# Kernel optimization log

Hardware: AMD Instinct MI355X
Metric: run time of the kernel (lower is better)

## Reference

```python
import jax, jax.numpy as jnp
import numpy as np
from jax import lax

LEAK = 0.01   # nn.LeakyReLU default negative slope
EPS = 1e-5    # BatchNorm2d eps


def _conv(x, w, b, stride, pad):
    # torch Conv2d, NCHW / OIHW
    y = lax.conv_general_dilated(x, w, (stride, stride), [(pad, pad), (pad, pad)],
                                 dimension_numbers=('NCHW', 'OIHW', 'NCHW'))
    return y + b[None, :, None, None]


def _bn_lrelu(x, g, b):
    # BatchNorm2d in training mode (torch default): batch statistics over (N,H,W)
    m = jnp.mean(x, axis=(0, 2, 3), keepdims=True)
    v = jnp.var(x, axis=(0, 2, 3), keepdims=True)
    xn = (x - m) * lax.rsqrt(v + EPS) * g[None, :, None, None] + b[None, :, None, None]
    return jnp.where(xn >= 0, xn, LEAK * xn)


def _convt(x, w, b):
    # ConvTranspose2d with stride == kernel_size, padding=0: non-overlapping
    # k x k expansion of every pixel -> expressible as one einsum + reshape.
    # w: (Cin, Cout, k, k) (torch ConvTranspose2d layout)
    B, C, H, W = x.shape
    _, Co, k, _ = w.shape
    y = jnp.einsum('bchw,coij->bohiwj', x, w).reshape(B, Co, H * k, W * k)
    return y + b[None, :, None, None]


def setup_inputs() -> dict:
    key = jax.random.key(0)
    ks = iter(jax.random.split(key, 64))
    def rn(shape, s=0.05):
        return jax.random.normal(next(ks), shape, dtype=jnp.float32) * s
    d = {}
    d['x'] = jax.random.normal(next(ks), (16, 3, 128, 128), dtype=jnp.float32)
    enc_shapes = [(64, 3, 4, 4), (128, 64, 4, 4), (256, 128, 4, 4), (256, 256, 4, 4)]
    for i, s in enumerate(enc_shapes):
        d[f'enc_w{i}'] = rn(s)
        d[f'enc_b{i}'] = jnp.zeros((s[0],), jnp.float32)
    for i, c in enumerate([64, 128, 256]):
        d[f'ebn_g{i}'] = jnp.ones((c,), jnp.float32)
        d[f'ebn_b{i}'] = jnp.zeros((c,), jnp.float32)
    d['codebook'] = rn((512, 256), 1.0)  # (codebook_size, latent_dim)
    dec_shapes = [(256, 128, 4, 4), (128, 64, 2, 2), (64, 32, 2, 2)]
    for i, s in enumerate(dec_shapes):
        d[f'dec_w{i}'] = rn(s)
        d[f'dec_b{i}'] = jnp.zeros((s[1],), jnp.float32)
        d[f'dbn_g{i}'] = jnp.ones((s[1],), jnp.float32)
        d[f'dbn_b{i}'] = jnp.zeros((s[1],), jnp.float32)
    d['dec_w3'] = rn((3, 32, 1, 1))
    d['dec_b3'] = jnp.zeros((3,), jnp.float32)
    return d


def reference(x,
              enc_w0, enc_b0, ebn_g0, ebn_b0,
              enc_w1, enc_b1, ebn_g1, ebn_b1,
              enc_w2, enc_b2, ebn_g2, ebn_b2,
              enc_w3, enc_b3,
              codebook,
              dec_w0, dec_b0, dbn_g0, dbn_b0,
              dec_w1, dec_b1, dbn_g1, dbn_b1,
              dec_w2, dec_b2, dbn_g2, dbn_b2,
              dec_w3, dec_b3):
    # ---- encoder ----
    h = _bn_lrelu(_conv(x, enc_w0, enc_b0, 2, 1), ebn_g0, ebn_b0)   # (B,64,64,64)
    h = _bn_lrelu(_conv(h, enc_w1, enc_b1, 2, 1), ebn_g1, ebn_b1)   # (B,128,32,32)
    h = _bn_lrelu(_conv(h, enc_w2, enc_b2, 2, 1), ebn_g2, ebn_b2)   # (B,256,16,16)
    z = _conv(h, enc_w3, enc_b3, 2, 1)                               # (B,256,8,8)

    # ---- vector quantizer ----
    B, C, H, W = z.shape
    zf = z.transpose(0, 2, 3, 1).reshape(-1, C)                      # (BHW, C)
    # squared L2 distances to every codebook entry
    d2 = (jnp.sum(zf * zf, axis=-1, keepdims=True)
          - 2.0 * zf @ codebook.T
          + jnp.sum(codebook * codebook, axis=-1)[None, :])          # (BHW, K)
    idx = jnp.argmin(d2, axis=-1)                                    # (BHW,)
    min_d = jnp.min(d2, axis=-1)
    q = codebook[idx]                                                # (BHW, C)
    commitment_loss = jnp.mean((lax.stop_gradient(q) - zf) ** 2)
    codebook_loss = jnp.mean((q - lax.stop_gradient(zf)) ** 2)
    q_st = zf + lax.stop_gradient(q - zf)                            # straight-through
    qz = q_st.reshape(B, H, W, C).transpose(0, 3, 1, 2)              # (B,256,8,8)

    # ---- decoder ----
    h = _bn_lrelu(_convt(qz, dec_w0, dec_b0), dbn_g0, dbn_b0)        # (B,128,32,32)
    h = _bn_lrelu(_convt(h, dec_w1, dec_b1), dbn_g1, dbn_b1)         # (B,64,64,64)
    h = _bn_lrelu(_convt(h, dec_w2, dec_b2), dbn_g2, dbn_b2)         # (B,32,128,128)
    out = jnp.tanh(jnp.einsum('bchw,oc->bohw', h, dec_w3[:, :, 0, 0])
                   + dec_b3[None, :, None, None])                    # (B,3,128,128)

    return (out, commitment_loss, codebook_loss,
            idx.reshape(B, H, W), min_d.reshape(B, H, W))
```

## Files before the change

### kernel.cpp

```cpp
#include <hip/hip_runtime.h>
#include <math.h>

#define LEAK 0.01f

typedef __bf16 bf16x8 __attribute__((ext_vector_type(8)));
typedef float f32x4 __attribute__((ext_vector_type(4)));
typedef unsigned short ushort;
typedef unsigned int uint32;

struct HL { ushort h, l; };

__device__ inline HL split_bf16(float x) {
    unsigned u = __float_as_uint(x);
    unsigned hr = (u + 0x7FFFu + ((u >> 16) & 1u)) >> 16;
    float fh = __uint_as_float(hr << 16);
    float r = x - fh;
    unsigned v = __float_as_uint(r);
    unsigned lr = (v + 0x7FFFu + ((v >> 16) & 1u)) >> 16;
    HL out; out.h = (ushort)hr; out.l = (ushort)lr;
    return out;
}

template<int MODE>
__device__ inline void stage_load(float (&pv)[2][4], const float* __restrict__ Bf,
                                  int kbase, int n0, int tid,
                                  int Ci, int Hin, int Ho, int lgHo, int lgHW) {
#pragma unroll
    for (int r = 0; r < 2; ++r) {
        int g = r * 256 + tid;
        int nl = g >> 3, kg = g & 7;
        int n = n0 + nl;
        if (MODE == 0) {
            int k4 = kbase + (kg << 2);
            int ic = k4 >> 4, kh = (k4 >> 2) & 3;
            int ow = n & (Ho - 1), oh = (n >> lgHo) & (Ho - 1), b = n >> (lgHo + lgHo);
            int ih = oh * 2 - 1 + kh;
            int ihc = ih < 0 ? 0 : (ih >= Hin ? Hin - 1 : ih);
            int iwb = ow * 2 - 1;
            size_t base = ((size_t)(b * Ci + ic) * Hin + ihc) * Hin;
#pragma unroll
            for (int e = 0; e < 4; ++e) {
                int iw = iwb + e;
                int iwc = iw < 0 ? 0 : (iw >= Hin ? Hin - 1 : iw);
                pv[r][e] = Bf[base + iwc];
            }
        } else {
            int c = kbase + (kg << 2);
            int b = n >> lgHW, hw = n & ((1 << lgHW) - 1);
            size_t base = (((size_t)(b * Ci + c)) << lgHW) + hw;
            size_t str = (size_t)1 << lgHW;
#pragma unroll
            for (int e = 0; e < 4; ++e) pv[r][e] = Bf[base + e * str];
        }
    }
}

template<int MODE>
__global__ __launch_bounds__(256, 3) void gemm_mfma(
    const ushort* __restrict__ Ah, const ushort* __restrict__ Al,
    const float* __restrict__ Bf,
    const float* __restrict__ bnt, const float* __restrict__ gamma,
    const float* __restrict__ beta, float invN, int chanShift,
    const float* __restrict__ bias, float* __restrict__ P,
    int Mtiles, int Ntiles, int K, int Kslice, int KS, int outSize,
    int Ci, int Hin, int Co, int Ho, int lgHo,
    int lgHW, int lgHin, int lgCo, int lgk,
    float* __restrict__ statsBnt)
{
    __shared__ __align__(16) uint32 Bsp[64 * 36];
    __shared__ float scs[256], shs[256];

    int bid = blockIdx.x;
    int ntile = bid % Ntiles; bid /= Ntiles;
    int mtile = bid % Mtiles;
    int ks = bid / Mtiles;
    int tid = threadIdx.x;
    int lane = tid & 63, w = tid >> 6;
    int quad = lane >> 4, tl = lane & 15;
    int n0 = ntile << 6, m0 = mtile << 7, k0 = ks * Kslice;
    int Kt = K >> 5;

    bool useBN = (bnt != nullptr);
    int c0 = k0 >> chanShift;
    if (useBN) {
        int nch = Kslice >> chanShift;
        for (int c = tid; c < nch; c += 256) {
            float m = bnt[(c0 + c) * 2] * invN;
            float var = bnt[(c0 + c) * 2 + 1] * invN - m * m;
            float scale = gamma[c0 + c] * rsqrtf(var + 1e-5f);
            scs[c] = scale;
            shs[c] = beta[c0 + c] - m * scale;
        }
    }
    __syncthreads();

    f32x4 zero4 = {0.f, 0.f, 0.f, 0.f};
    f32x4 acc[2][4];
#pragma unroll
    for (int mt = 0; mt < 2; ++mt)
#pragma unroll
        for (int nt = 0; nt < 4; ++nt) acc[mt][nt] = zero4;

    float pv[2][4];
    stage_load<MODE>(pv, Bf, k0, n0, tid, Ci, Hin, Ho, lgHo, lgHW);

    for (int kc = 0; kc < Kslice; kc += 32) {
        int kbase = k0 + kc;
        int kt = kbase >> 5;
#pragma unroll
        for (int r = 0; r < 2; ++r) {
            int g = r * 256 + tid;
            int nl = g >> 3, kg = g & 7;
            int k4 = kbase + (kg << 2);
            uint32 pk[4];
            if (MODE == 0) {
                int ic = k4 >> 4, kh = (k4 >> 2) & 3;
                int n = n0 + nl;
                int ow = n & (Ho - 1), oh = (n >> lgHo) & (Ho - 1);
                int ih = oh * 2 - 1 + kh;
                bool rowok = (unsigned)ih < (unsigned)Hin;
                int iwb = ow * 2 - 1;
                float sc_ = useBN ? scs[ic - c0] : 0.f;
                float sh_ = useBN ? shs[ic - c0] : 0.f;
#pragma unroll
                for (int e = 0; e < 4; ++e) {
                    int iw = iwb + e;
                    bool ok = rowok && ((unsigned)iw < (unsigned)Hin);
                    float f = pv[r][e];
                    if (useBN) { f = f * sc_ + sh_; f = f >= 0.f ? f : LEAK * f; }
                    if (!ok) f = 0.f;
                    HL s = split_bf16(f);
                    pk[e] = ((uint32)s.h << 16) | s.l;
                }
            } else {
#pragma unroll
                for (int e = 0; e < 4; ++e) {
                    float f = pv[r][e];
                    if (useBN) {
                        int lc = k4 + e - k0;
                        f = f * scs[lc] + shs[lc];
                        f = f >= 0.f ? f : LEAK * f;
                    }
                    HL s = split_bf16(f);
                    pk[e] = ((uint32)s.h << 16) | s.l;
                }
            }
            *(uint4*)&Bsp[nl * 36 + (kg << 2)] = make_uint4(pk[0], pk[1], pk[2], pk[3]);
        }
        __syncthreads();

        bool more = (kc + 32) < Kslice;
        float pvn[2][4];
        if (more) stage_load<MODE>(pvn, Bf, kbase + 32, n0, tid, Ci, Hin, Ho, lgHo, lgHW);

        bf16x8 afh[2], afl[2];
#pragma unroll
        for (int mt = 0; mt < 2; ++mt) {
            int mtAbs = (m0 >> 4) + (w << 1) + mt;
            size_t abase = (((size_t)mtAbs * Kt + kt) << 6) + lane;
            afh[mt] = *(const bf16x8*)(Ah + abase * 8);
            afl[mt] = *(const bf16x8*)(Al + abase * 8);
        }
        bf16x8 bfh[4], bfl[4];
#pragma unroll
        for (int nt = 0; nt < 4; ++nt) {
            int base = ((nt << 4) + tl) * 36 + (quad << 3);
            uint4 ua = *(const uint4*)&Bsp[base];
            uint4 ub = *(const uint4*)&Bsp[base + 4];
            union { uint32 u[4]; bf16x8 v; } H, L;
            H.u[0] = __builtin_amdgcn_perm(ua.y, ua.x, 0x07060302u);
            H.u[1] = __builtin_amdgcn_perm(ua.w, ua.z, 0x07060302u);
            H.u[2] = __builtin_amdgcn_perm(ub.y, ub.x, 0x07060302u);
            H.u[3] = __builtin_amdgcn_perm(ub.w, ub.z, 0x07060302u);
            L.u[0] = __builtin_amdgcn_perm(ua.y, ua.x, 0x05040100u);
            L.u[1] = __builtin_amdgcn_perm(ua.w, ua.z, 0x05040100u);
            L.u[2] = __builtin_amdgcn_perm(ub.y, ub.x, 0x05040100u);
            L.u[3] = __builtin_amdgcn_perm(ub.w, ub.z, 0x05040100u);
            bfh[nt] = H.v; bfl[nt] = L.v;
        }
#pragma unroll
        for (int mt = 0; mt < 2; ++mt)
#pragma unroll
            for (int nt = 0; nt < 4; ++nt) {
                acc[mt][nt] = __builtin_amdgcn_mfma_f32_16x16x32_bf16(afh[mt], bfh[nt], acc[mt][nt], 0, 0, 0);
                acc[mt][nt] = __builtin_amdgcn_mfma_f32_16x16x32_bf16(afh[mt], bfl[nt], acc[mt][nt], 0, 0, 0);
                acc[mt][nt] = __builtin_amdgcn_mfma_f32_16x16x32_bf16(afl[mt], bfh[nt], acc[mt][nt], 0, 0, 0);
            }
        __syncthreads();
        if (more) {
#pragma unroll
            for (int r = 0; r < 2; ++r)
#pragma unroll
                for (int e = 0; e < 4; ++e) pv[r][e] = pvn[r][e];
        }
    }

    float* dst = P + (size_t)ks * outSize;
    if (MODE == 0) {
#pragma unroll
        for (int nt = 0; nt < 4; ++nt) {
            int n = n0 + (nt << 4) + tl;
            int ow = n & (Ho - 1), oh = (n >> lgHo) & (Ho - 1), b = n >> (lgHo + lgHo);
#pragma unroll
            for (int mt = 0; mt < 2; ++mt) {
                int mb = m0 + (w << 5) + (mt << 4) + (quad << 2);
#pragma unroll
                for (int r = 0; r < 4; ++r) {
                    int oc = mb + r;
                    float v = acc[mt][nt][r];
                    if (KS == 1) v += bias[oc];
                    dst[((size_t)(b * Co + oc) * Ho + oh) * Ho + ow] = v;
                }
            }
        }
    } else {
        bool doStats = (statsBnt != nullptr);
        if (doStats) {
            if (tid < 2 * Co) scs[tid] = 0.f;
            __syncthreads();
        }
        int kf = 1 << lgk;
        int Ho2 = Hin << lgk;
        float ssum[2][4] = {{0.f,0.f,0.f,0.f},{0.f,0.f,0.f,0.f}};
        float ssq [2][4] = {{0.f,0.f,0.f,0.f},{0.f,0.f,0.f,0.f}};
#pragma unroll
        for (int nt = 0; nt < 4; ++nt) {
            int n = n0 + (nt << 4) + tl;
            int b = n >> lgHW, hw = n & ((1 << lgHW) - 1);
            int h = hw >> lgHin, wp = hw & (Hin - 1);
#pragma unroll
            for (int mt = 0; mt < 2; ++mt) {
                int mb = m0 + (w << 5) + (mt << 4) + (quad << 2);
#pragma unroll
                for (int r = 0; r < 4; ++r) {
                    int m = mb + r;
                    int o = m & (Co - 1), ij = m >> lgCo;
                    int ii = ij >> lgk, jj = ij & (kf - 1);
                    float v = acc[mt][nt][r];
                    if (KS == 1) v += bias[o];
                    if (doStats) { ssum[mt][r] += v; ssq[mt][r] += v * v; }
                    dst[((size_t)(b * Co + o) * Ho2 + (h << lgk) + ii) * Ho2 + (wp << lgk) + jj] = v;
                }
            }
        }
        if (doStats) {
#pragma unroll
            for (int mt = 0; mt < 2; ++mt)
#pragma unroll
                for (int r = 0; r < 4; ++r) {
                    float s = ssum[mt][r], q2 = ssq[mt][r];
#pragma unroll
                    for (int m2 = 1; m2 < 16; m2 <<= 1) {
                        s  += __shfl_xor(s,  m2);
                        q2 += __shfl_xor(q2, m2);
                    }
                    if (tl == 0) {
                        int m = m0 + (w << 5) + (mt << 4) + (quad << 2) + r;
                        int o = m & (Co - 1);
                        atomicAdd(&scs[o * 2],     s);
                        atomicAdd(&scs[o * 2 + 1], q2);
                    }
                }
            __syncthreads();
            if (tid < 2 * Co) atomicAdd(&statsBnt[tid], scs[tid]);
        }
    }
}

__device__ inline int fragaddr(int m, int k, int K) {
    return ((((m >> 4) * (K >> 5) + (k >> 5)) << 9) | (((k >> 3) & 3) << 7) | ((m & 15) << 3) | (k & 7));
}

#define OUT_CL   786432
#define OUT_CB   786433
#define OUT_IDX  786434
#define OUT_MIND 787458

__global__ void prologue(const float* __restrict__ w1, const float* __restrict__ w2,
                         const float* __restrict__ w3, const float* __restrict__ d0,
                         const float* __restrict__ d1, const float* __restrict__ d2,
                         ushort* __restrict__ WH, ushort* __restrict__ WL,
                         const float* __restrict__ cb, float* __restrict__ cbT,
                         float* __restrict__ bnt, float* __restrict__ dout) {
    int blk = blockIdx.x;
    int tid = threadIdx.x;
    if (blk < 24) {
        bnt[blk * 256 + tid] = 0.f;
        if (blk == 0 && tid < 2) dout[OUT_CL + tid] = 0.f;
        return;
    }
    if (blk < 536) {
        int idx = (blk - 24) * 256 + tid;
        int k = idx & 511, c = idx >> 9;
        cbT[idx] = cb[k * 256 + c];
        return;
    }
    int idx = (blk - 536) * 256 + tid;
    if (idx >= 2269184) return;
    float v; int dst;
    if (idx < 131072) {
        int m = idx >> 10, k = idx & 1023;
        v = w1[idx];
        dst = fragaddr(m, k, 1024);
    } else if (idx < 655360) {
        int i = idx - 131072;
        int m = i >> 11, k = i & 2047;
        v = w2[i];
        dst = 131072 + fragaddr(m, k, 2048);
    } else if (idx < 1703936) {
        int i = idx - 655360;
        int m = i >> 12, k = i & 4095;
        v = w3[i];
        dst = 655360 + fragaddr(m, k, 4096);
    } else if (idx < 2228224) {
        int i = idx - 1703936;
        int m = i >> 8, c = i & 255;
        int o = m & 127, ij = m >> 7;
        v = d0[((size_t)c * 128 + o) * 16 + ij];
        dst = 1703936 + fragaddr(m, c, 256);
    } else if (idx < 2260992) {
        int i = idx - 2228224;
        int m = i >> 7, c = i & 127;
        int o = m & 63, ij = m >> 6;
        v = d1[((size_t)c * 64 + o) * 4 + ij];
        dst = 2228224 + fragaddr(m, c, 128);
    } else {
        int i = idx - 2260992;
        int m = i >> 6, c = i & 63;
        int o = m & 31, ij = m >> 5;
        v = d2[((size_t)c * 32 + o) * 4 + ij];
        dst = 2260992 + fragaddr(m, c, 64);
    }
    HL s = split_bf16(v);
    WH[dst] = s.h; WL[dst] = s.l;
}

template<int OCT>
__global__ __launch_bounds__(256) void conv4x4(
    const float* __restrict__ x, const float* __restrict__ w,
    const float* __restrict__ bias, float* __restrict__ P,
    float* __restrict__ bnt,
    int B, int Ci, int Hin, int Co, int Ho)
{
    __shared__ float cst[4][2 * OCT];
    int ogn = Co / OCT;
    int ntile = (B * Ho * Ho) >> 8;
    int bid = blockIdx.x;
    int tile = bid % ntile; bid /= ntile;
    int og = bid % ogn;
    int oc0 = og * OCT;

    int px = (tile << 8) + threadIdx.x;
    int ow = px % Ho; int t = px / Ho;
    int oh = t % Ho;  int b = t / Ho;

    int off[16]; float fm[16];
    int ih0 = oh * 2 - 1, iw0 = ow * 2 - 1;
#pragma unroll
    for (int kh = 0; kh < 4; ++kh)
#pragma unroll
        for (int kw = 0; kw < 4; ++kw) {
            int ih = ih0 + kh, iw = iw0 + kw;
            bool ok = (ih >= 0) && (ih < Hin) && (iw >= 0) && (iw < Hin);
            int ihc = ih < 0 ? 0 : (ih >= Hin ? Hin - 1 : ih);
            int iwc = iw < 0 ? 0 : (iw >= Hin ? Hin - 1 : iw);
            off[kh * 4 + kw] = ihc * Hin + iwc;
            fm[kh * 4 + kw] = ok ? 1.f : 0.f;
        }

    float acc[OCT];
#pragma unroll
    for (int u = 0; u < OCT; ++u) acc[u] = bias[oc0 + u];

    const float* xc = x + (size_t)b * Ci * Hin * Hin;
    const float* wi = w + (size_t)oc0 * Ci * 16;
    int HinHin = Hin * Hin;
    for (int ic = 0; ic < Ci; ++ic) {
        float xv[16];
#pragma unroll
        for (int q = 0; q < 16; ++q) xv[q] = xc[off[q]] * fm[q];
#pragma unroll
        for (int u = 0; u < OCT; ++u) {
            const float* wo = wi + (size_t)u * Ci * 16;
            float a = acc[u];
#pragma unroll
            for (int q = 0; q < 16; ++q) a += xv[q] * wo[q];
            acc[u] = a;
        }
        xc += HinHin;
        wi += 16;
    }
    size_t obase = (((size_t)b * Co + oc0) * Ho + oh) * Ho + ow;
    size_t opl = (size_t)Ho * Ho;
#pragma unroll
    for (int u = 0; u < OCT; ++u) P[obase + u * opl] = acc[u];

    float sv[OCT], qv[OCT];
#pragma unroll
    for (int u = 0; u < OCT; ++u) { sv[u] = acc[u]; qv[u] = acc[u] * acc[u]; }
#pragma unroll
    for (int m2 = 1; m2 < 64; m2 <<= 1)
#pragma unroll
        for (int u = 0; u < OCT; ++u) {
            sv[u] += __shfl_xor(sv[u], m2);
            qv[u] += __shfl_xor(qv[u], m2);
        }
    int lane = threadIdx.x & 63, wv = threadIdx.x >> 6;
    if (lane == 0) {
#pragma unroll
        for (int u = 0; u < OCT; ++u) { cst[wv][u * 2] = sv[u]; cst[wv][u * 2 + 1] = qv[u]; }
    }
    __syncthreads();
    if (threadIdx.x < 2 * OCT) {
        float v = cst[0][threadIdx.x] + cst[1][threadIdx.x] + cst[2][threadIdx.x] + cst[3][threadIdx.x];
        atomicAdd(&bnt[(oc0 + (threadIdx.x >> 1)) * 2 + (threadIdx.x & 1)], v);
    }
}

__global__ void reduce_bias4(const float4* __restrict__ P, const float* __restrict__ bias,
                             float4* __restrict__ y, int outSize4, int KS, int Co, int HW4) {
    int i = blockIdx.x * 256 + threadIdx.x;
    if (i >= outSize4) return;
    float bv = bias[(i / HW4) % Co];
    float4 s = make_float4(bv, bv, bv, bv);
    for (int ks = 0; ks < KS; ++ks) {
        float4 p = P[(size_t)ks * outSize4 + i];
        s.x += p.x; s.y += p.y; s.z += p.z; s.w += p.w;
    }
    y[i] = s;
}

__global__ void reduce_bias_stats4(const float4* __restrict__ P, const float* __restrict__ bias,
                                   float4* __restrict__ y, float* __restrict__ bnt,
                                   int outSize4, int KS, int Co, int HW4, int nch) {
    int tid = threadIdx.x;
    int i = blockIdx.x * 256 + tid;
    int c = (i / HW4) % Co;
    float bv = bias[c];
    float4 s = make_float4(bv, bv, bv, bv);
    for (int ks = 0; ks < KS; ++ks) {
        float4 p = P[(size_t)ks * outSize4 + i];
        s.x += p.x; s.y += p.y; s.z += p.z; s.w += p.w;
    }
    y[i] = s;
    float ls  = s.x + s.y + s.z + s.w;
    float ls2 = s.x * s.x + s.y * s.y + s.z * s.z + s.w * s.w;
    __shared__ float as[16], aq[16];
    if (tid < 16) { as[tid] = 0.f; aq[tid] = 0.f; }
    __syncthreads();
    int c0 = ((blockIdx.x * 256) / HW4) % Co;
    atomicAdd(&as[c - c0], ls);
    atomicAdd(&aq[c - c0], ls2);
    __syncthreads();
    if (tid < nch) {
        atomicAdd(&bnt[(c0 + tid) * 2],     as[tid]);
        atomicAdd(&bnt[(c0 + tid) * 2 + 1], aq[tid]);
    }
}

__global__ void vq_main(const float* __restrict__ z, const float* __restrict__ cbT,
                        const float* __restrict__ cb,
                        float* __restrict__ q, float* __restrict__ dout) {
    int r0 = blockIdx.x * 4;
    int tid = threadIdx.x;
    int lane = tid & 63, w = tid >> 6;

    __shared__ __align__(16) float zT[256][4];
    __shared__ float wred[4][4];
    __shared__ float zn2s[4];
    __shared__ float wbd[4][4];
    __shared__ int   wbi[4][4];
    __shared__ int   bestsh[4];
    __shared__ float bestd[4];

    int b = r0 >> 6, s0 = r0 & 63;
    float4 zv = *(const float4*)&z[((size_t)(b * 256 + tid)) * 64 + s0];
    *(float4*)&zT[tid][0] = zv;

    float p0 = zv.x * zv.x, p1 = zv.y * zv.y, p2 = zv.z * zv.z, p3 = zv.w * zv.w;
#pragma unroll
    for (int m2 = 1; m2 < 64; m2 <<= 1) {
        p0 += __shfl_xor(p0, m2); p1 += __shfl_xor(p1, m2);
        p2 += __shfl_xor(p2, m2); p3 += __shfl_xor(p3, m2);
    }
    if (lane == 0) { wred[w][0] = p0; wred[w][1] = p1; wred[w][2] = p2; wred[w][3] = p3; }
    __syncthreads();
    if (tid < 4) zn2s[tid] = wred[0][tid] + wred[1][tid] + wred[2][tid] + wred[3][tid];
    __syncthreads();

    float d0[4], d1[4];
#pragma unroll
    for (int rr = 0; rr < 4; ++rr) { d0[rr] = 0.f; d1[rr] = 0.f; }
    float cn0 = 0.f, cn1 = 0.f;
#pragma unroll 4
    for (int c = 0; c < 256; ++c) {
        float cv0 = cbT[c * 512 + tid];
        float cv1 = cbT[c * 512 + 256 + tid];
        cn0 += cv0 * cv0;
        cn1 += cv1 * cv1;
        float4 za = *(const float4*)&zT[c][0];
        d0[0] += za.x * cv0; d1[0] += za.x * cv1;
        d0[1] += za.y * cv0; d1[1] += za.y * cv1;
        d0[2] += za.z * cv0; d1[2] += za.z * cv1;
        d0[3] += za.w * cv0; d1[3] += za.w * cv1;
    }

#pragma unroll
    for (int rr = 0; rr < 4; ++rr) {
        float dist0 = zn2s[rr] - 2.f * d0[rr] + cn0;
        float dist1 = zn2s[rr] - 2.f * d1[rr] + cn1;
        float bd = dist0; int bi = tid;
        if (dist1 < bd) { bd = dist1; bi = tid + 256; }
#pragma unroll
        for (int m2 = 1; m2 < 64; m2 <<= 1) {
            float od = __shfl_xor(bd, m2); int oi = __shfl_xor(bi, m2);
            if (od < bd || (od == bd && oi < bi)) { bd = od; bi = oi; }
        }
        if (lane == 0) { wbd[w][rr] = bd; wbi[w][rr] = bi; }
    }
    __syncthreads();
    if (tid < 4) {
        float bd = wbd[0][tid]; int bi = wbi[0][tid];
#pragma unroll
        for (int ww = 1; ww < 4; ++ww) {
            float od = wbd[ww][tid]; int oi = wbi[ww][tid];
            if (od < bd || (od == bd && oi < bi)) { bd = od; bi = oi; }
        }
        bestsh[tid] = bi; bestd[tid] = bd;
        dout[OUT_IDX + r0 + tid]  = (float)bi;
        dout[OUT_MIND + r0 + tid] = bd;
    }
    __syncthreads();

    float4 qv;
    qv.x = cb[(size_t)bestsh[0] * 256 + tid];
    qv.y = cb[(size_t)bestsh[1] * 256 + tid];
    qv.z = cb[(size_t)bestsh[2] * 256 + tid];
    qv.w = cb[(size_t)bestsh[3] * 256 + tid];
    *(float4*)&q[((size_t)(b * 256 + tid)) * 64 + s0] = qv;
    if (tid == 0) {
        float ls = (bestd[0] + bestd[1] + bestd[2] + bestd[3]) * (1.f / 262144.f);
        atomicAdd(&dout[OUT_CL], ls);
        atomicAdd(&dout[OUT_CB], ls);
    }
}

__global__ void final_conv_tanh(const float* __restrict__ hbuf, const float* __restrict__ bnt,
                                const float* __restrict__ g, const float* __restrict__ bt,
                                const float* __restrict__ w3, const float* __restrict__ b3,
                                float* __restrict__ out) {
    __shared__ float sc[32], sh[32], sw[96];
    int tid = threadIdx.x;
    if (tid < 32) {
        float m = bnt[tid * 2] * (1.f / 262144.f);
        float var = bnt[tid * 2 + 1] * (1.f / 262144.f) - m * m;
        float scale = g[tid] * rsqrtf(var + 1e-5f);
        sc[tid] = scale;
        sh[tid] = bt[tid] - m * scale;
    }
    if (tid < 96) sw[tid] = w3[tid];
    __syncthreads();
    int idx = blockIdx.x * 256 + tid;
    int hw4 = idx & 4095;
    int b   = idx >> 12;
    const float4* hp = (const float4*)hbuf + ((size_t)b * 32) * 4096 + hw4;
    float b0 = b3[0], b1 = b3[1], b2 = b3[2];
    float4 a0 = make_float4(b0, b0, b0, b0);
    float4 a1 = make_float4(b1, b1, b1, b1);
    float4 a2 = make_float4(b2, b2, b2, b2);
#pragma unroll 8
    for (int c = 0; c < 32; ++c) {
        float4 v = hp[(size_t)c * 4096];
        float scv = sc[c], shv = sh[c];
        float vx = v.x * scv + shv; vx = vx >= 0.f ? vx : LEAK * vx;
        float vy = v.y * scv + shv; vy = vy >= 0.f ? vy : LEAK * vy;
        float vz = v.z * scv + shv; vz = vz >= 0.f ? vz : LEAK * vz;
        float vw = v.w * scv + shv; vw = vw >= 0.f ? vw : LEAK * vw;
        float w0 = sw[c], w1 = sw[32 + c], w2 = sw[64 + c];
        a0.x += vx * w0; a0.y += vy * w0; a0.z += vz * w0; a0.w += vw * w0;
        a1.x += vx * w1; a1.y += vy * w1; a1.z += vz * w1; a1.w += vw * w1;
        a2.x += vx * w2; a2.y += vy * w2; a2.z += vz * w2; a2.w += vw * w2;
    }
    float4* op = (float4*)out;
    size_t ob = ((size_t)b * 3) * 4096 + hw4;
    op[ob]            = make_float4(tanhf(a0.x), tanhf(a0.y), tanhf(a0.z), tanhf(a0.w));
    op[ob + 4096]     = make_float4(tanhf(a1.x), tanhf(a1.y), tanhf(a1.z), tanhf(a1.w));
    op[ob + 2 * 4096] = make_float4(tanhf(a2.x), tanhf(a2.y), tanhf(a2.z), tanhf(a2.w));
}

extern "C" void kernel_launch(void* const* d_in, const int* in_sizes, int n_in,
                              void* d_out, int out_size, void* d_ws, size_t ws_size,
                              hipStream_t stream) {
    const float* x      = (const float*)d_in[0];
    const float* enc_w0 = (const float*)d_in[1];
    const float* enc_b0 = (const float*)d_in[2];
    const float* enc_w1 = (const float*)d_in[3];
    const float* enc_b1 = (const float*)d_in[4];
    const float* enc_w2 = (const float*)d_in[5];
    const float* enc_b2 = (const float*)d_in[6];
    const float* enc_w3 = (const float*)d_in[7];
    const float* enc_b3 = (const float*)d_in[8];
    const float* ebn_g0 = (const float*)d_in[9];
    const float* ebn_b0 = (const float*)d_in[10];
    const float* ebn_g1 = (const float*)d_in[11];
    const float* ebn_b1 = (const float*)d_in[12];
    const float* ebn_g2 = (const float*)d_in[13];
    const float* ebn_b2 = (const float*)d_in[14];
    const float* cb     = (const float*)d_in[15];
    const float* dec_w0 = (const float*)d_in[16];
    const float* dec_b0 = (const float*)d_in[17];
    const float* dbn_g0 = (const float*)d_in[18];
    const float* dbn_b0 = (const float*)d_in[19];
    const float* dec_w1 = (const float*)d_in[20];
    const float* dec_b1 = (const float*)d_in[21];
    const float* dbn_g1 = (const float*)d_in[22];
    const float* dbn_b1 = (const float*)d_in[23];
    const float* dec_w2 = (const float*)d_in[24];
    const float* dec_b2 = (const float*)d_in[25];
    const float* dbn_g2 = (const float*)d_in[26];
    const float* dbn_b2 = (const float*)d_in[27];
    const float* dec_w3 = (const float*)d_in[28];
    const float* dec_b3 = (const float*)d_in[29];

    float* out = (float*)d_out;
    float* ws  = (float*)d_ws;

    float*  Y0   = ws;
    float*  Y1   = ws + 4194304;
    float*  Y2   = ws + 6291456;
    float*  Z    = ws + 7340032;
    float*  Q    = ws + 7602176;
    ushort* WH   = (ushort*)(ws + 7864320);
    ushort* WL   = (ushort*)(ws + 8998912);
    float*  CBT  = ws + 10133504;
    float*  BNT  = ws + 10264576;
    float*  PART = ws + 10270720;
    float*  D0   = ws + 18659328;
    float*  D1   = ws + 20756480;
    float*  D2   = ws + 24950784;

    dim3 blk(256);

    prologue<<<9400, blk, 0, stream>>>(enc_w1, enc_w2, enc_w3, dec_w0, dec_w1, dec_w2,
                                       WH, WL, cb, CBT, BNT, out);

    conv4x4<8><<<2048, blk, 0, stream>>>(x, enc_w0, enc_b0, Y0, BNT, 16, 3, 128, 64, 64);

    gemm_mfma<0><<<512, blk, 0, stream>>>(WH, WL, Y0,
        BNT, ebn_g0, ebn_b0, 1.f / 65536.f, 4, enc_b1, PART,
        1, 256, 1024, 512, 2, 2097152, 64, 64, 128, 32, 5, 0, 0, 0, 0, nullptr);
    reduce_bias_stats4<<<2048, blk, 0, stream>>>((const float4*)PART, enc_b1, (float4*)Y1,
                                                 BNT + 1024, 524288, 2, 128, 256, 1);

    gemm_mfma<0><<<512, blk, 0, stream>>>(WH + 131072, WL + 131072, Y1,
        BNT + 1024, ebn_g1, ebn_b1, 1.f / 16384.f, 4, enc_b2, PART,
        2, 64, 2048, 512, 4, 1048576, 128, 32, 256, 16, 4, 0, 0, 0, 0, nullptr);
    reduce_bias_stats4<<<1024, blk, 0, stream>>>((const float4*)PART, enc_b2, (float4*)Y2,
                                                 BNT + 2048, 262144, 4, 256, 64, 4);

    gemm_mfma<0><<<512, blk, 0, stream>>>(WH + 655360, WL + 655360, Y2,
        BNT + 2048, ebn_g2, ebn_b2, 1.f / 4096.f, 4, enc_b3, PART,
        2, 16, 4096, 256, 16, 262144, 256, 16, 256, 8, 3, 0, 0, 0, 0, nullptr);
    reduce_bias4<<<256, blk, 0, stream>>>((const float4*)PART, enc_b3, (float4*)Z, 65536, 16, 256, 16);

    vq_main<<<256, blk, 0, stream>>>(Z, CBT, cb, Q, out);

    gemm_mfma<1><<<512, blk, 0, stream>>>(WH + 1703936, WL + 1703936, Q,
        nullptr, nullptr, nullptr, 0.f, 0, dec_b0, PART,
        16, 16, 256, 128, 2, 2097152, 256, 8, 128, 0, 0, 6, 3, 7, 2, nullptr);
    reduce_bias_stats4<<<2048, blk, 0, stream>>>((const float4*)PART, dec_b0, (float4*)D0,
                                                 BNT + 3072, 524288, 2, 128, 256, 1);

    gemm_mfma<1><<<512, blk, 0, stream>>>(WH + 2228224, WL + 2228224, D0,
        BNT + 3072, dbn_g0, dbn_b0, 1.f / 16384.f, 0, dec_b1, D1,
        2, 256, 128, 128, 1, 0, 128, 32, 64, 0, 0, 10, 5, 6, 1, BNT + 4096);

    gemm_mfma<1><<<1024, blk, 0, stream>>>(WH + 2260992, WL + 2260992, D1,
        BNT + 4096, dbn_g1, dbn_b1, 1.f / 65536.f, 0, dec_b2, D2,
        1, 1024, 64, 64, 1, 0, 64, 64, 32, 0, 0, 12, 6, 5, 1, BNT + 5120);

    final_conv_tanh<<<256, blk, 0, stream>>>(D2, BNT + 5120, dbn_g2, dbn_b2, dec_w3, dec_b3, out);
}
```

Before: 413.1 us.

## Fuse first conv into prologue and drop split-K reduce kernels

Merges the first encoder conv into the prologue launch and has it write per-tile BN partial sums instead of doing global atomics. The next GEMM reduces those partials itself. Adds an MT template so some GEMMs use 64-row M tiles without split-K and compute BN stats in their epilogue, removing two reduce_bias_stats passes. The final encoder split-K sum is folded into vq_main, which removes another reduce kernel and cuts launches and intermediate traffic. The trade-off is smaller tiles and less K-parallelism in the affected GEMMs, plus partial-sum reduction overhead in every block.

```diff
diff --git a/kernel.cpp b/kernel.cpp
--- a/kernel.cpp
+++ b/kernel.cpp
@@ -55,7 +55,7 @@
     }
 }
 
-template<int MODE>
+template<int MODE, int MT>
 __global__ __launch_bounds__(256, 3) void gemm_mfma(
     const ushort* __restrict__ Ah, const ushort* __restrict__ Al,
     const float* __restrict__ Bf,
@@ -65,7 +65,7 @@
     int Mtiles, int Ntiles, int K, int Kslice, int KS, int outSize,
     int Ci, int Hin, int Co, int Ho, int lgHo,
     int lgHW, int lgHin, int lgCo, int lgk,
-    float* __restrict__ statsBnt)
+    float* __restrict__ statsBnt, const float* __restrict__ bnPart)
 {
     __shared__ __align__(16) uint32 Bsp[64 * 36];
     __shared__ float scs[256], shs[256];
@@ -77,12 +77,31 @@
     int tid = threadIdx.x;
     int lane = tid & 63, w = tid >> 6;
     int quad = lane >> 4, tl = lane & 15;
-    int n0 = ntile << 6, m0 = mtile << 7, k0 = ks * Kslice;
+    int n0 = ntile << 6, m0 = mtile << (MT == 2 ? 7 : 6), k0 = ks * Kslice;
     int Kt = K >> 5;
 
-    bool useBN = (bnt != nullptr);
+    bool useBN = (bnt != nullptr) || (bnPart != nullptr);
     int c0 = k0 >> chanShift;
-    if (useBN) {
+    if (bnPart != nullptr) {
+        int c = tid >> 2, qq = tid & 3;
+        const float2* pp2 = (const float2*)(bnPart + c * 512) + qq * 64;
+        float s = 0.f, s2 = 0.f;
+#pragma unroll 8
+        for (int p = 0; p < 64; ++p) { float2 v = pp2[p]; s += v.x; s2 += v.y; }
+        scs[tid] = s; shs[tid] = s2;
+        __syncthreads();
+        float scale = 0.f, shift = 0.f;
+        if (tid < 64) {
+            float st = scs[tid * 4] + scs[tid * 4 + 1] + scs[tid * 4 + 2] + scs[tid * 4 + 3];
+            float qt = shs[tid * 4] + shs[tid * 4 + 1] + shs[tid * 4 + 2] + shs[tid * 4 + 3];
+            float m = st * invN;
+            float var = qt * invN - m * m;
+            scale = gamma[tid] * rsqrtf(var + 1e-5f);
+            shift = beta[tid] - m * scale;
+        }
+        __syncthreads();
+        if (tid < 64) { scs[tid] = scale; shs[tid] = shift; }
+    } else if (bnt != nullptr) {
         int nch = Kslice >> chanShift;
         for (int c = tid; c < nch; c += 256) {
             float m = bnt[(c0 + c) * 2] * invN;
@@ -95,9 +114,9 @@
     __syncthreads();
 
     f32x4 zero4 = {0.f, 0.f, 0.f, 0.f};
-    f32x4 acc[2][4];
-#pragma unroll
-    for (int mt = 0; mt < 2; ++mt)
+    f32x4 acc[MT][4];
+#pragma unroll
+    for (int mt = 0; mt < MT; ++mt)
 #pragma unroll
         for (int nt = 0; nt < 4; ++nt) acc[mt][nt] = zero4;
 
@@ -153,10 +172,10 @@
         float pvn[2][4];
         if (more) stage_load<MODE>(pvn, Bf, kbase + 32, n0, tid, Ci, Hin, Ho, lgHo, lgHW);
 
-        bf16x8 afh[2], afl[2];
-#pragma unroll
-        for (int mt = 0; mt < 2; ++mt) {
-            int mtAbs = (m0 >> 4) + (w << 1) + mt;
+        bf16x8 afh[MT], afl[MT];
+#pragma unroll
+        for (int mt = 0; mt < MT; ++mt) {
+            int mtAbs = (m0 >> 4) + w * MT + mt;
             size_t abase = (((size_t)mtAbs * Kt + kt) << 6) + lane;
             afh[mt] = *(const bf16x8*)(Ah + abase * 8);
             afl[mt] = *(const bf16x8*)(Al + abase * 8);
@@ -179,7 +198,7 @@
             bfh[nt] = H.v; bfl[nt] = L.v;
         }
 #pragma unroll
-        for (int mt = 0; mt < 2; ++mt)
+        for (int mt = 0; mt < MT; ++mt)
 #pragma unroll
             for (int nt = 0; nt < 4; ++nt) {
                 acc[mt][nt] = __builtin_amdgcn_mfma_f32_16x16x32_bf16(afh[mt], bfh[nt], acc[mt][nt], 0, 0, 0);
@@ -195,6 +214,13 @@
         }
     }
 
+    bool doStats = (statsBnt != nullptr);
+    if (doStats) {
+        if (tid < 2 * Co) scs[tid] = 0.f;
+        __syncthreads();
+    }
+    float ssum[MT][4] = {};
+    float ssq [MT][4] = {};
     float* dst = P + (size_t)ks * outSize;
     if (MODE == 0) {
 #pragma unroll
@@ -202,35 +228,29 @@
             int n = n0 + (nt << 4) + tl;
             int ow = n & (Ho - 1), oh = (n >> lgHo) & (Ho - 1), b = n >> (lgHo + lgHo);
 #pragma unroll
-            for (int mt = 0; mt < 2; ++mt) {
-                int mb = m0 + (w << 5) + (mt << 4) + (quad << 2);
+            for (int mt = 0; mt < MT; ++mt) {
+                int mb = m0 + ((w * MT + mt) << 4) + (quad << 2);
 #pragma unroll
                 for (int r = 0; r < 4; ++r) {
                     int oc = mb + r;
                     float v = acc[mt][nt][r];
                     if (KS == 1) v += bias[oc];
+                    if (doStats) { ssum[mt][r] += v; ssq[mt][r] += v * v; }
                     dst[((size_t)(b * Co + oc) * Ho + oh) * Ho + ow] = v;
                 }
             }
         }
     } else {
-        bool doStats = (statsBnt != nullptr);
-        if (doStats) {
-            if (tid < 2 * Co) scs[tid] = 0.f;
-            __syncthreads();
-        }
         int kf = 1 << lgk;
         int Ho2 = Hin << lgk;
-        float ssum[2][4] = {{0.f,0.f,0.f,0.f},{0.f,0.f,0.f,0.f}};
-        float ssq [2][4] = {{0.f,0.f,0.f,0.f},{0.f,0.f,0.f,0.f}};
 #pragma unroll
         for (int nt = 0; nt < 4; ++nt) {
             int n = n0 + (nt << 4) + tl;
             int b = n >> lgHW, hw = n & ((1 << lgHW) - 1);
             int h = hw >> lgHin, wp = hw & (Hin - 1);
 #pragma unroll
-            for (int mt = 0; mt < 2; ++mt) {
-                int mb = m0 + (w << 5) + (mt << 4) + (quad << 2);
+            for (int mt = 0; mt < MT; ++mt) {
+                int mb = m0 + ((w * MT + mt) << 4) + (quad << 2);
 #pragma unroll
                 for (int r = 0; r < 4; ++r) {
                     int m = mb + r;
@@ -243,27 +263,27 @@
                 }
             }
         }
-        if (doStats) {
-#pragma unroll
-            for (int mt = 0; mt < 2; ++mt)
-#pragma unroll
-                for (int r = 0; r < 4; ++r) {
-                    float s = ssum[mt][r], q2 = ssq[mt][r];
-#pragma unroll
-                    for (int m2 = 1; m2 < 16; m2 <<= 1) {
-                        s  += __shfl_xor(s,  m2);
-                        q2 += __shfl_xor(q2, m2);
-                    }
-                    if (tl == 0) {
-                        int m = m0 + (w << 5) + (mt << 4) + (quad << 2) + r;
-                        int o = m & (Co - 1);
-                        atomicAdd(&scs[o * 2],     s);
-                        atomicAdd(&scs[o * 2 + 1], q2);
-                    }
+    }
+    if (doStats) {
+#pragma unroll
+        for (int mt = 0; mt < MT; ++mt)
+#pragma unroll
+            for (int r = 0; r < 4; ++r) {
+                float s = ssum[mt][r], q2 = ssq[mt][r];
+#pragma unroll
+                for (int m2 = 1; m2 < 16; m2 <<= 1) {
+                    s  += __shfl_xor(s,  m2);
+                    q2 += __shfl_xor(q2, m2);
                 }
-            __syncthreads();
-            if (tid < 2 * Co) atomicAdd(&statsBnt[tid], scs[tid]);
-        }
+                if (tl == 0) {
+                    int m = m0 + ((w * MT + mt) << 4) + (quad << 2) + r;
+                    int o = (MODE == 0) ? m : (m & (Co - 1));
+                    atomicAdd(&scs[o * 2],     s);
+                    atomicAdd(&scs[o * 2 + 1], q2);
+                }
+            }
+        __syncthreads();
+        if (tid < 2 * Co) atomicAdd(&statsBnt[tid], scs[tid]);
     }
 }
 
@@ -275,13 +295,95 @@
 #define OUT_CB   786433
 #define OUT_IDX  786434
 #define OUT_MIND 787458
+
+__device__ void conv_body(int bid, int tid,
+                          const float* __restrict__ x, const float* __restrict__ w,
+                          const float* __restrict__ bias, float* __restrict__ P,
+                          float* __restrict__ pst, float (&cst)[4][16])
+{
+    const int Ci = 3, Hin = 128, Co = 64, Ho = 64, OCT = 8;
+    int ntile = (16 * Ho * Ho) >> 8;
+    int tile = bid % ntile;
+    int og = bid / ntile;
+    int oc0 = og * OCT;
+
+    int px = (tile << 8) + tid;
+    int ow = px % Ho; int t = px / Ho;
+    int oh = t % Ho;  int b = t / Ho;
+
+    int off[16]; float fm[16];
+    int ih0 = oh * 2 - 1, iw0 = ow * 2 - 1;
+#pragma unroll
+    for (int kh = 0; kh < 4; ++kh)
+#pragma unroll
+        for (int kw = 0; kw < 4; ++kw) {
+            int ih = ih0 + kh, iw = iw0 + kw;
+            bool ok = (ih >= 0) && (ih < Hin) && (iw >= 0) && (iw < Hin);
+            int ihc = ih < 0 ? 0 : (ih >= Hin ? Hin - 1 : ih);
+            int iwc = iw < 0 ? 0 : (iw >= Hin ? Hin - 1 : iw);
+            off[kh * 4 + kw] = ihc * Hin + iwc;
+            fm[kh * 4 + kw] = ok ? 1.f : 0.f;
+        }
+
+    float acc[OCT];
+#pragma unroll
+    for (int u = 0; u < OCT; ++u) acc[u] = bias[oc0 + u];
+
+    const float* xc = x + (size_t)b * Ci * Hin * Hin;
+    const float* wi = w + (size_t)oc0 * Ci * 16;
+    int HinHin = Hin * Hin;
+    for (int ic = 0; ic < Ci; ++ic) {
+        float xv[16];
+#pragma unroll
+        for (int q = 0; q < 16; ++q) xv[q] = xc[off[q]] * fm[q];
+#pragma unroll
+        for (int u = 0; u < OCT; ++u) {
+            const float* wo = wi + (size_t)u * Ci * 16;
+            float a = acc[u];
+#pragma unroll
+            for (int q = 0; q < 16; ++q) a += xv[q] * wo[q];
+            acc[u] = a;
+        }
+        xc += HinHin;
+        wi += 16;
+    }
+    size_t obase = (((size_t)b * Co + oc0) * Ho + oh) * Ho + ow;
+    size_t opl = (size_t)Ho * Ho;
+#pragma unroll
+    for (int u = 0; u < OCT; ++u) P[obase + u * opl] = acc[u];
+
+    float sv[OCT], qv[OCT];
+#pragma unroll
+    for (int u = 0; u < OCT; ++u) { sv[u] = acc[u]; qv[u] = acc[u] * acc[u]; }
+#pragma unroll
+    for (int m2 = 1; m2 < 64; m2 <<= 1)
+#pragma unroll
+        for (int u = 0; u < OCT; ++u) {
+            sv[u] += __shfl_xor(sv[u], m2);
+            qv[u] += __shfl_xor(qv[u], m2);
+        }
+    int lane = tid & 63, wv = tid >> 6;
+    if (lane == 0) {
+#pragma unroll
+        for (int u = 0; u < OCT; ++u) { cst[wv][u * 2] = sv[u]; cst[wv][u * 2 + 1] = qv[u]; }
+    }
+    __syncthreads();
+    if (tid < 2 * OCT) {
+        float v = cst[0][tid] + cst[1][tid] + cst[2][tid] + cst[3][tid];
+        pst[(oc0 + (tid >> 1)) * 512 + tile * 2 + (tid & 1)] = v;
+    }
+}
 
 __global__ void prologue(const float* __restrict__ w1, const float* __restrict__ w2,
                          const float* __restrict__ w3, const float* __restrict__ d0,
                          const float* __restrict__ d1, const float* __restrict__ d2,
                          ushort* __restrict__ WH, ushort* __restrict__ WL,
                          const float* __restrict__ cb, float* __restrict__ cbT,
-                         float* __restrict__ bnt, float* __restrict__ dout) {
+                         float* __restrict__ bnt, float* __restrict__ dout,
+                         const float* __restrict__ x, const float* __restrict__ w0,
+                         const float* __restrict__ b0, float* __restrict__ Y0,
+                         float* __restrict__ pst) {
+    __shared__ float cst[4][16];
     int blk = blockIdx.x;
     int tid = threadIdx.x;
     if (blk < 24) {
@@ -293,6 +395,10 @@
         int idx = (blk - 24) * 256 + tid;
         int k = idx & 511, c = idx >> 9;
         cbT[idx] = cb[k * 256 + c];
+        return;
+    }
+    if (blk >= 9400) {
+        conv_body(blk - 9400, tid, x, w0, b0, Y0, pst, cst);
         return;
     }
     int idx = (blk - 536) * 256 + tid;
@@ -335,101 +441,6 @@
     WH[dst] = s.h; WL[dst] = s.l;
 }
 
-template<int OCT>
-__global__ __launch_bounds__(256) void conv4x4(
-    const float* __restrict__ x, const float* __restrict__ w,
-    const float* __restrict__ bias, float* __restrict__ P,
-    float* __restrict__ bnt,
-    int B, int Ci, int Hin, int Co, int Ho)
-{
-    __shared__ float cst[4][2 * OCT];
-    int ogn = Co / OCT;
-    int ntile = (B * Ho * Ho) >> 8;
-    int bid = blockIdx.x;
-    int tile = bid % ntile; bid /= ntile;
-    int og = bid % ogn;
-    int oc0 = og * OCT;
-
-    int px = (tile << 8) + threadIdx.x;
-    int ow = px % Ho; int t = px / Ho;
-    int oh = t % Ho;  int b = t / Ho;
-
-    int off[16]; float fm[16];
-    int ih0 = oh * 2 - 1, iw0 = ow * 2 - 1;
-#pragma unroll
-    for (int kh = 0; kh < 4; ++kh)
-#pragma unroll
-        for (int kw = 0; kw < 4; ++kw) {
-            int ih = ih0 + kh, iw = iw0 + kw;
-            bool ok = (ih >= 0) && (ih < Hin) && (iw >= 0) && (iw < Hin);
-            int ihc = ih < 0 ? 0 : (ih >= Hin ? Hin - 1 : ih);
-            int iwc = iw < 0 ? 0 : (iw >= Hin ? Hin - 1 : iw);
-            off[kh * 4 + kw] = ihc * Hin + iwc;
-            fm[kh * 4 + kw] = ok ? 1.f : 0.f;
-        }
-
-    float acc[OCT];
-#pragma unroll
-    for (int u = 0; u < OCT; ++u) acc[u] = bias[oc0 + u];
-
-    const float* xc = x + (size_t)b * Ci * Hin * Hin;
-    const float* wi = w + (size_t)oc0 * Ci * 16;
-    int HinHin = Hin * Hin;
-    for (int ic = 0; ic < Ci; ++ic) {
-        float xv[16];
-#pragma unroll
-        for (int q = 0; q < 16; ++q) xv[q] = xc[off[q]] * fm[q];
-#pragma unroll
-        for (int u = 0; u < OCT; ++u) {
-            const float* wo = wi + (size_t)u * Ci * 16;
-            float a = acc[u];
-#pragma unroll
-            for (int q = 0; q < 16; ++q) a += xv[q] * wo[q];
-            acc[u] = a;
-        }
-        xc += HinHin;
-        wi += 16;
-    }
-    size_t obase = (((size_t)b * Co + oc0) * Ho + oh) * Ho + ow;
-    size_t opl = (size_t)Ho * Ho;
-#pragma unroll
-    for (int u = 0; u < OCT; ++u) P[obase + u * opl] = acc[u];
-
-    float sv[OCT], qv[OCT];
-#pragma unroll
-    for (int u = 0; u < OCT; ++u) { sv[u] = acc[u]; qv[u] = acc[u] * acc[u]; }
-#pragma unroll
-    for (int m2 = 1; m2 < 64; m2 <<= 1)
-#pragma unroll
-        for (int u = 0; u < OCT; ++u) {
-            sv[u] += __shfl_xor(sv[u], m2);
-            qv[u] += __shfl_xor(qv[u], m2);
-        }
-    int lane = threadIdx.x & 63, wv = threadIdx.x >> 6;
-    if (lane == 0) {
-#pragma unroll
-        for (int u = 0; u < OCT; ++u) { cst[wv][u * 2] = sv[u]; cst[wv][u * 2 + 1] = qv[u]; }
-    }
-    __syncthreads();
-    if (threadIdx.x < 2 * OCT) {
-        float v = cst[0][threadIdx.x] + cst[1][threadIdx.x] + cst[2][threadIdx.x] + cst[3][threadIdx.x];
-        atomicAdd(&bnt[(oc0 + (threadIdx.x >> 1)) * 2 + (threadIdx.x & 1)], v);
-    }
-}
-
-__global__ void reduce_bias4(const float4* __restrict__ P, const float* __restrict__ bias,
-                             float4* __restrict__ y, int outSize4, int KS, int Co, int HW4) {
-    int i = blockIdx.x * 256 + threadIdx.x;
-    if (i >= outSize4) return;
-    float bv = bias[(i / HW4) % Co];
-    float4 s = make_float4(bv, bv, bv, bv);
-    for (int ks = 0; ks < KS; ++ks) {
-        float4 p = P[(size_t)ks * outSize4 + i];
-        s.x += p.x; s.y += p.y; s.z += p.z; s.w += p.w;
-    }
-    y[i] = s;
-}
-
 __global__ void reduce_bias_stats4(const float4* __restrict__ P, const float* __restrict__ bias,
                                    float4* __restrict__ y, float* __restrict__ bnt,
                                    int outSize4, int KS, int Co, int HW4, int nch) {
@@ -458,8 +469,8 @@
     }
 }
 
-__global__ void vq_main(const float* __restrict__ z, const float* __restrict__ cbT,
-                        const float* __restrict__ cb,
+__global__ void vq_main(const float* __restrict__ Pz, const float* __restrict__ b3,
+                        const float* __restrict__ cbT, const float* __restrict__ cb,
                         float* __restrict__ q, float* __restrict__ dout) {
     int r0 = blockIdx.x * 4;
     int tid = threadIdx.x;
@@ -474,7 +485,15 @@
     __shared__ float bestd[4];
 
     int b = r0 >> 6, s0 = r0 & 63;
-    float4 zv = *(const float4*)&z[((size_t)(b * 256 + tid)) * 64 + s0];
+    size_t zi = ((size_t)(b * 256 + tid)) * 64 + s0;
+    float bv = b3[tid];
+    float4 zv = make_float4(bv, bv, bv, bv);
+    const float4* pp = (const float4*)Pz + (zi >> 2);
+#pragma unroll
+    for (int ks = 0; ks < 16; ++ks) {
+        float4 p = pp[(size_t)ks * 65536];
+        zv.x += p.x; zv.y += p.y; zv.z += p.z; zv.w += p.w;
+    }
     *(float4*)&zT[tid][0] = zv;
 
     float p0 = zv.x * zv.x, p1 = zv.y * zv.y, p2 = zv.z * zv.z, p3 = zv.w * zv.w;
@@ -628,7 +647,7 @@
     float*  Y0   = ws;
     float*  Y1   = ws + 4194304;
     float*  Y2   = ws + 6291456;
-    float*  Z    = ws + 7340032;
+    float*  PST  = ws + 7340032;
     float*  Q    = ws + 7602176;
     ushort* WH   = (ushort*)(ws + 7864320);
     ushort* WL   = (ushort*)(ws + 8998912);
@@ -641,43 +660,37 @@
 
     dim3 blk(256);
 
-    prologue<<<9400, blk, 0, stream>>>(enc_w1, enc_w2, enc_w3, dec_w0, dec_w1, dec_w2,
-                                       WH, WL, cb, CBT, BNT, out);
-
-    conv4x4<8><<<2048, blk, 0, stream>>>(x, enc_w0, enc_b0, Y0, BNT, 16, 3, 128, 64, 64);
-
-    gemm_mfma<0><<<512, blk, 0, stream>>>(WH, WL, Y0,
-        BNT, ebn_g0, ebn_b0, 1.f / 65536.f, 4, enc_b1, PART,
-        1, 256, 1024, 512, 2, 2097152, 64, 64, 128, 32, 5, 0, 0, 0, 0, nullptr);
-    reduce_bias_stats4<<<2048, blk, 0, stream>>>((const float4*)PART, enc_b1, (float4*)Y1,
-                                                 BNT + 1024, 524288, 2, 128, 256, 1);
-
-    gemm_mfma<0><<<512, blk, 0, stream>>>(WH + 131072, WL + 131072, Y1,
+    prologue<<<11448, blk, 0, stream>>>(enc_w1, enc_w2, enc_w3, dec_w0, dec_w1, dec_w2,
+                                        WH, WL, cb, CBT, BNT, out,
+                                        x, enc_w0, enc_b0, Y0, PST);
+
+    gemm_mfma<0, 1><<<512, blk, 0, stream>>>(WH, WL, Y0,
+        nullptr, ebn_g0, ebn_b0, 1.f / 65536.f, 4, enc_b1, Y1,
+        2, 256, 1024, 1024, 1, 0, 64, 64, 128, 32, 5, 0, 0, 0, 0, BNT + 1024, PST);
+
+    gemm_mfma<0, 2><<<512, blk, 0, stream>>>(WH + 131072, WL + 131072, Y1,
         BNT + 1024, ebn_g1, ebn_b1, 1.f / 16384.f, 4, enc_b2, PART,
-        2, 64, 2048, 512, 4, 1048576, 128, 32, 256, 16, 4, 0, 0, 0, 0, nullptr);
+        2, 64, 2048, 512, 4, 1048576, 128, 32, 256, 16, 4, 0, 0, 0, 0, nullptr, nullptr);
     reduce_bias_stats4<<<1024, blk, 0, stream>>>((const float4*)PART, enc_b2, (float4*)Y2,
                                                  BNT + 2048, 262144, 4, 256, 64, 4);
 
-    gemm_mfma<0><<<512, blk, 0, stream>>>(WH + 655360, WL + 655360, Y2,
+    gemm_mfma<0, 2><<<512, blk, 0, stream>>>(WH + 655360, WL + 655360, Y2,
         BNT + 2048, ebn_g2, ebn_b2, 1.f / 4096.f, 4, enc_b3, PART,
-        2, 16, 4096, 256, 16, 262144, 256, 16, 256, 8, 3, 0, 0, 0, 0, nullptr);
-    reduce_bias4<<<256, blk, 0, stream>>>((const float4*)PART, enc_b3, (float4*)Z, 65536, 16, 256, 16);
-
-    vq_main<<<256, blk, 0, stream>>>(Z, CBT, cb, Q, out);
-
-    gemm_mfma<1><<<512, blk, 0, stream>>>(WH + 1703936, WL + 1703936, Q,
-        nullptr, nullptr, nullptr, 0.f, 0, dec_b0, PART,
-        16, 16, 256, 128, 2, 2097152, 256, 8, 128, 0, 0, 6, 3, 7, 2, nullptr);
-    reduce_bias_stats4<<<2048, blk, 0, stream>>>((const float4*)PART, dec_b0, (float4*)D0,
-                                                 BNT + 3072, 524288, 2, 128, 256, 1);
-
-    gemm_mfma<1><<<512, blk, 0, stream>>>(WH + 2228224, WL + 2228224, D0,
+        2, 16, 4096, 256, 16, 262144, 256, 16, 256, 8, 3, 0, 0, 0, 0, nullptr, nullptr);
+
+    vq_main<<<256, blk, 0, stream>>>(PART, enc_b3, CBT, cb, Q, out);
+
+    gemm_mfma<1, 1><<<512, blk, 0, stream>>>(WH + 1703936, WL + 1703936, Q,
+        nullptr, nullptr, nullptr, 0.f, 0, dec_b0, D0,
+        32, 16, 256, 256, 1, 0, 256, 8, 128, 0, 0, 6, 3, 7, 2, BNT + 3072, nullptr);
+
+    gemm_mfma<1, 2><<<512, blk, 0, stream>>>(WH + 2228224, WL + 2228224, D0,
         BNT + 3072, dbn_g0, dbn_b0, 1.f / 16384.f, 0, dec_b1, D1,
-        2, 256, 128, 128, 1, 0, 128, 32, 64, 0, 0, 10, 5, 6, 1, BNT + 4096);
-
-    gemm_mfma<1><<<1024, blk, 0, stream>>>(WH + 2260992, WL + 2260992, D1,
+        2, 256, 128, 128, 1, 0, 128, 32, 64, 0, 0, 10, 5, 6, 1, BNT + 4096, nullptr);
+
+    gemm_mfma<1, 2><<<1024, blk, 0, stream>>>(WH + 2260992, WL + 2260992, D1,
         BNT + 4096, dbn_g1, dbn_b1, 1.f / 65536.f, 0, dec_b2, D2,
-        1, 1024, 64, 64, 1, 0, 64, 64, 32, 0, 0, 12, 6, 5, 1, BNT + 5120);
+        1, 1024, 64, 64, 1, 0, 64, 64, 32, 0, 0, 12, 6, 5, 1, BNT + 5120, nullptr);
 
     final_conv_tanh<<<256, blk, 0, stream>>>(D2, BNT + 5120, dbn_g2, dbn_b2, dec_w3, dec_b3, out);
 }
```

After: 443.1 us. +7.3%, slower.
